# Kernel tuning notes

Measured on AMD Instinct MI355X. Metric: run time of the kernel, lower is better.

Reference implementation:

```python
import jax, jax.numpy as jnp
import numpy as np

TEMPERATURE = 0.5


def setup_inputs() -> dict:
    key = jax.random.key(0)
    k1, k2 = jax.random.split(key)
    N, Z = 4096, 2048
    z1 = jax.random.normal(k1, (N, Z), dtype=jnp.float32)
    z2 = jax.random.normal(k2, (N, Z), dtype=jnp.float32)
    return {"z1": z1, "z2": z2}


def reference(z1, z2):
    # NT-Xent loss. Original torch code: normalize, build full 2Nx2N cosine-sim
    # matrix, prepend the positive pair column, cross-entropy with label 0.
    # Mathematically, per-row CE with the positive prepended and the self-sim
    # removed equals: logsumexp over the row excluding the diagonal, minus the
    # positive logit.  (cosine_similarity on already-normalized vectors is a
    # plain dot product, so normalization is applied once.)
    n, _ = z1.shape
    a = z1 / jnp.linalg.norm(z1, axis=1, keepdims=True)  # [N, Z]
    b = z2 / jnp.linalg.norm(z2, axis=1, keepdims=True)  # [N, Z]
    reps = jnp.concatenate([a, b], axis=0)               # [2N, Z]
    logits = jnp.matmul(reps, reps.T) / TEMPERATURE      # [2N, 2N]
    NEG_INF = jnp.float32(-1e9)  # mask self-similarity (excluded from CE denom)
    logits = jnp.where(jnp.eye(2 * n, dtype=bool), NEG_INF, logits)
    pos = jnp.sum(a * b, axis=1) / TEMPERATURE           # [N] positive logits
    pos = jnp.concatenate([pos, pos])                    # [2N]
    lse = jax.nn.logsumexp(logits, axis=1)               # [2N]
    # sum of CE over 2N rows, divided by 2N  == mean
    return jnp.mean(lse - pos)
```

## Files before the change

### kernel.cpp

```cpp
#include <hip/hip_runtime.h>
#include <stdint.h>

#define N_ROWS 4096
#define Z_DIM  2048
#define TOT    8192
#define TILE   128
#define RBYTES (Z_DIM / 2)
#define BKE    256
#define KBYT   (BKE / 2)
#define NITER  (Z_DIM / BKE)
#define NT     (TOT / TILE)
#define NBLK   (NT * (NT + 1) / 2)
#define INV_T  2.0f
#define SCL4   64.0f

typedef __attribute__((ext_vector_type(4))) int   intx4;
typedef __attribute__((ext_vector_type(8))) int   intx8;
typedef __attribute__((ext_vector_type(4))) float floatx4;

__device__ __forceinline__ unsigned int f2fp4(float v) {
    float a = fabsf(v);
    unsigned int c = (a >= 0.25f) + (a >= 0.75f) + (a >= 1.25f) + (a >= 1.75f)
                   + (a >= 2.5f)  + (a >= 3.5f)  + (a >= 5.0f);
    return c | (v < 0.f ? 8u : 0u);
}

#define GLOAD16(g, l)                                                   \
    __builtin_amdgcn_global_load_lds(                                   \
        (const __attribute__((address_space(1))) unsigned int*)(g),     \
        (__attribute__((address_space(3))) unsigned int*)(l), 16, 0, 0)

__global__ __launch_bounds__(256) void normalize_kernel(
    const float* __restrict__ z1, const float* __restrict__ z2,
    unsigned char* __restrict__ reps, float* __restrict__ pos,
    float* __restrict__ rowsum)
{
    const int row  = blockIdx.x;
    const int tid  = threadIdx.x;
    const int lane = tid & 63, wave = tid >> 6;

    if (row < TOT / 256) rowsum[row * 256 + tid] = 0.f;

    const float4* p1 = (const float4*)(z1 + (size_t)row * Z_DIM);
    const float4* p2 = (const float4*)(z2 + (size_t)row * Z_DIM);
    float4 x0 = p1[tid * 2], x1 = p1[tid * 2 + 1];
    float4 y0 = p2[tid * 2], y1 = p2[tid * 2 + 1];

    float s1 = x0.x*x0.x + x0.y*x0.y + x0.z*x0.z + x0.w*x0.w
             + x1.x*x1.x + x1.y*x1.y + x1.z*x1.z + x1.w*x1.w;
    float s2 = y0.x*y0.x + y0.y*y0.y + y0.z*y0.z + y0.w*y0.w
             + y1.x*y1.x + y1.y*y1.y + y1.z*y1.z + y1.w*y1.w;
    float dd = x0.x*y0.x + x0.y*y0.y + x0.z*y0.z + x0.w*y0.w
             + x1.x*y1.x + x1.y*y1.y + x1.z*y1.z + x1.w*y1.w;

    #pragma unroll
    for (int m = 1; m < 64; m <<= 1) {
        s1 += __shfl_xor(s1, m);
        s2 += __shfl_xor(s2, m);
        dd += __shfl_xor(dd, m);
    }
    __shared__ float red[3][4];
    if (lane == 0) { red[0][wave] = s1; red[1][wave] = s2; red[2][wave] = dd; }
    __syncthreads();
    s1 = red[0][0] + red[0][1] + red[0][2] + red[0][3];
    s2 = red[1][0] + red[1][1] + red[1][2] + red[1][3];
    dd = red[2][0] + red[2][1] + red[2][2] + red[2][3];

    const float inv1 = rsqrtf(s1), inv2 = rsqrtf(s2);
    if (tid == 0) {
        float p = dd * inv1 * inv2 * INV_T;
        pos[row] = p;
        pos[row + N_ROWS] = p;
    }

    const float a = inv1 * SCL4, b = inv2 * SCL4;
    unsigned int pa =  f2fp4(x0.x * a)        | (f2fp4(x0.y * a) << 4)
                    | (f2fp4(x0.z * a) << 8)  | (f2fp4(x0.w * a) << 12)
                    | (f2fp4(x1.x * a) << 16) | (f2fp4(x1.y * a) << 20)
                    | (f2fp4(x1.z * a) << 24) | (f2fp4(x1.w * a) << 28);
    unsigned int pb =  f2fp4(y0.x * b)        | (f2fp4(y0.y * b) << 4)
                    | (f2fp4(y0.z * b) << 8)  | (f2fp4(y0.w * b) << 12)
                    | (f2fp4(y1.x * b) << 16) | (f2fp4(y1.y * b) << 20)
                    | (f2fp4(y1.z * b) << 24) | (f2fp4(y1.w * b) << 28);
    *(unsigned int*)(reps + (size_t)row * RBYTES + tid * 4) = pa;
    *(unsigned int*)(reps + (size_t)(N_ROWS + row) * RBYTES + tid * 4) = pb;
}

__global__ __launch_bounds__(256) void simclr_gemm(
    const unsigned char* __restrict__ reps, float* __restrict__ rowsum)
{
    __shared__ __align__(16) unsigned char L[2][2][16384];

    const int t = blockIdx.x;
    int r = (int)((sqrtf(8.0f * (float)t + 1.0f) - 1.0f) * 0.5f);
    while ((r + 1) * (r + 2) / 2 <= t) ++r;
    while (r * (r + 1) / 2 > t) --r;
    const int bi = t - r * (r + 1) / 2;
    const int bj = r;
    const bool diag = (bi == bj);

    const int tid  = threadIdx.x;
    const int lane = tid & 63, wave = tid >> 6;
    const int wr = wave >> 1, wc = wave & 1;
    const int quad = lane >> 4, l16 = lane & 15;
    const int sw   = l16 & 3;
    const int row0 = bi * TILE, col0 = bj * TILE;

    floatx4 acc[4][4];
    #pragma unroll
    for (int i = 0; i < 4; ++i)
        #pragma unroll
        for (int j = 0; j < 4; ++j)
            acc[i][j] = floatx4{0.f, 0.f, 0.f, 0.f};

    const int r_lo = tid >> 2, slot = tid & 3;
    const unsigned char* gA[4]; const unsigned char* gB[4]; int lofs[4];
    #pragma unroll
    for (int p = 0; p < 4; ++p) {
        const int rw = (p & 1) * 64 + r_lo;
        const int kc = (p >> 1) * 4 + (slot ^ (r_lo & 3));
        gA[p] = reps + (size_t)(row0 + rw) * RBYTES + kc * 16;
        gB[p] = reps + (size_t)(col0 + rw) * RBYTES + kc * 16;
        lofs[p] = p * 4096 + tid * 16;
    }

    #pragma unroll
    for (int p = 0; p < 4; ++p) GLOAD16(gA[p], &L[0][0][lofs[p]]);
    #pragma unroll
    for (int p = 0; p < 4; ++p) GLOAD16(gB[p], &L[0][1][lofs[p]]);
    __syncthreads();

    for (int i = 0; i < NITER; ++i) {
        if (i + 1 < NITER) {
            const size_t ko = (size_t)(i + 1) * KBYT;
            const int buf = (i + 1) & 1;
            #pragma unroll
            for (int p = 0; p < 4; ++p) GLOAD16(gA[p] + ko, &L[buf][0][lofs[p]]);
            #pragma unroll
            for (int p = 0; p < 4; ++p) GLOAD16(gB[p] + ko, &L[buf][1][lofs[p]]);
        }
        const unsigned char* Ab = &L[i & 1][0][0];
        const unsigned char* Bb = &L[i & 1][1][0];

        intx8 af[2][4], bf[2][4];
        #pragma unroll
        for (int h = 0; h < 2; ++h) {
            #pragma unroll
            for (int f = 0; f < 4; ++f) {
                const int ra = h * 8192 + (wr * 64 + f * 16 + l16) * 64 + ((quad ^ sw) << 4);
                const int rb = h * 8192 + (wc * 64 + f * 16 + l16) * 64 + ((quad ^ sw) << 4);
                intx4 av = *(const intx4*)&Ab[ra];
                intx4 bv = *(const intx4*)&Bb[rb];
                af[h][f] = intx8{av[0], av[1], av[2], av[3], 0, 0, 0, 0};
                bf[h][f] = intx8{bv[0], bv[1], bv[2], bv[3], 0, 0, 0, 0};
            }
        }
        #pragma unroll
        for (int h = 0; h < 2; ++h)
            #pragma unroll
            for (int fi = 0; fi < 4; ++fi)
                #pragma unroll
                for (int j = 0; j < 4; ++j)
                    acc[fi][j] = __builtin_amdgcn_mfma_scale_f32_16x16x128_f8f6f4(
                        af[h][fi], bf[h][j], acc[fi][j],
                        4, 4,
                        0, 0x7F7F7F7Fu,
                        0, 0x7F7F7F7Fu);
        __syncthreads();
    }

    const float descale = INV_T / (SCL4 * SCL4);
    float scol[4] = {0.f, 0.f, 0.f, 0.f};
    #pragma unroll
    for (int fi = 0; fi < 4; ++fi) {
        const int rbase = row0 + wr * 64 + fi * 16 + quad * 4;
        float srow[4] = {0.f, 0.f, 0.f, 0.f};
        #pragma unroll
        for (int j = 0; j < 4; ++j) {
            const int c = col0 + wc * 64 + j * 16 + l16;
            #pragma unroll
            for (int rr = 0; rr < 4; ++rr) {
                float e = __expf(acc[fi][j][rr] * descale);
                if (diag && (rbase + rr == c)) e = 0.f;
                srow[rr] += e;
                scol[j]  += e;
            }
        }
        #pragma unroll
        for (int rr = 0; rr < 4; ++rr) {
            #pragma unroll
            for (int m = 1; m < 16; m <<= 1) srow[rr] += __shfl_xor(srow[rr], m);
        }
        if (l16 == 0) {
            #pragma unroll
            for (int rr = 0; rr < 4; ++rr)
                atomicAdd(&rowsum[rbase + rr], srow[rr]);
        }
    }
    if (!diag) {
        #pragma unroll
        for (int j = 0; j < 4; ++j) {
            scol[j] += __shfl_xor(scol[j], 16);
            scol[j] += __shfl_xor(scol[j], 32);
        }
        if (quad == 0) {
            #pragma unroll
            for (int j = 0; j < 4; ++j)
                atomicAdd(&rowsum[col0 + wc * 64 + j * 16 + l16], scol[j]);
        }
    }
}

__global__ __launch_bounds__(1024) void finalize_kernel(
    const float* __restrict__ rowsum, const float* __restrict__ pos,
    float* __restrict__ out)
{
    const int tid = threadIdx.x;
    const int lane = tid & 63, wave = tid >> 6;
    float s = 0.f;
    for (int r = tid; r < TOT; r += 1024) s += logf(rowsum[r]) - pos[r];
    #pragma unroll
    for (int m = 1; m < 64; m <<= 1) s += __shfl_xor(s, m);
    __shared__ float red[16];
    if (lane == 0) red[wave] = s;
    __syncthreads();
    if (tid == 0) {
        float t = 0.f;
        #pragma unroll
        for (int w = 0; w < 16; ++w) t += red[w];
        out[0] = t * (1.0f / TOT);
    }
}

extern "C" void kernel_launch(void* const* d_in, const int* in_sizes, int n_in,
                              void* d_out, int out_size, void* d_ws, size_t ws_size,
                              hipStream_t stream)
{
    const float* z1 = (const float*)d_in[0];
    const float* z2 = (const float*)d_in[1];
    float* out = (float*)d_out;

    char* w = (char*)d_ws;
    unsigned char* reps = (unsigned char*)w;
    float* pos    = (float*)(w + (size_t)TOT * RBYTES);
    float* rowsum = pos + TOT;

    normalize_kernel<<<N_ROWS, 256, 0, stream>>>(z1, z2, reps, pos, rowsum);
    simclr_gemm<<<NBLK, 256, 0, stream>>>(reps, rowsum);
    finalize_kernel<<<1, 1024, 0, stream>>>(rowsum, pos, out);
}
```

Measured before the change: 157.2 us.

## Switch GEMM to 32x32x64 FP4 MFMA with two-wave blocks and smaller K-step

Replaces the 16x16x128 scaled FP4 MFMA tiles with 32x32x64 ones. Each block now has 2 waves instead of 4, each wave computing a 128x64 slab, and the LDS K-step is halved to 128 elements, which halves shared memory per block. The aim is fewer, larger MFMA instructions with better operand reuse, and more resident blocks per CU. The cost is more accumulator registers per wave, twice as many K iterations and barriers, and a wider row reduction in the epilogue (16 values reduced across 32 lanes).

Result: slower. 188.8 us (+20.1%).

```diff
diff --git a/kernel.cpp b/kernel.cpp
--- a/kernel.cpp
+++ b/kernel.cpp
@@ -6,7 +6,7 @@
 #define TOT    8192
 #define TILE   128
 #define RBYTES (Z_DIM / 2)
-#define BKE    256
+#define BKE    128
 #define KBYT   (BKE / 2)
 #define NITER  (Z_DIM / BKE)
 #define NT     (TOT / TILE)
@@ -14,9 +14,9 @@
 #define INV_T  2.0f
 #define SCL4   64.0f
 
-typedef __attribute__((ext_vector_type(4))) int   intx4;
-typedef __attribute__((ext_vector_type(8))) int   intx8;
-typedef __attribute__((ext_vector_type(4))) float floatx4;
+typedef __attribute__((ext_vector_type(4)))  int   intx4;
+typedef __attribute__((ext_vector_type(8)))  int   intx8;
+typedef __attribute__((ext_vector_type(16))) float floatx16;
 
 __device__ __forceinline__ unsigned int f2fp4(float v) {
     float a = fabsf(v);
@@ -86,10 +86,10 @@
     *(unsigned int*)(reps + (size_t)(N_ROWS + row) * RBYTES + tid * 4) = pb;
 }
 
-__global__ __launch_bounds__(256) void simclr_gemm(
+__global__ __launch_bounds__(128) void simclr_gemm(
     const unsigned char* __restrict__ reps, float* __restrict__ rowsum)
 {
-    __shared__ __align__(16) unsigned char L[2][2][16384];
+    __shared__ __align__(16) unsigned char L[2][2][8192];
 
     const int t = blockIdx.x;
     int r = (int)((sqrtf(8.0f * (float)t + 1.0f) - 1.0f) * 0.5f);
@@ -101,33 +101,31 @@
 
     const int tid  = threadIdx.x;
     const int lane = tid & 63, wave = tid >> 6;
-    const int wr = wave >> 1, wc = wave & 1;
-    const int quad = lane >> 4, l16 = lane & 15;
-    const int sw   = l16 & 3;
+    const int l32  = lane & 31, half = lane >> 5;
     const int row0 = bi * TILE, col0 = bj * TILE;
 
-    floatx4 acc[4][4];
+    floatx16 acc[4][2];
     #pragma unroll
     for (int i = 0; i < 4; ++i)
         #pragma unroll
-        for (int j = 0; j < 4; ++j)
-            acc[i][j] = floatx4{0.f, 0.f, 0.f, 0.f};
-
-    const int r_lo = tid >> 2, slot = tid & 3;
+        for (int j = 0; j < 2; ++j)
+            #pragma unroll
+            for (int e = 0; e < 16; ++e) acc[i][j][e] = 0.f;
+
     const unsigned char* gA[4]; const unsigned char* gB[4]; int lofs[4];
     #pragma unroll
-    for (int p = 0; p < 4; ++p) {
-        const int rw = (p & 1) * 64 + r_lo;
-        const int kc = (p >> 1) * 4 + (slot ^ (r_lo & 3));
-        gA[p] = reps + (size_t)(row0 + rw) * RBYTES + kc * 16;
-        gB[p] = reps + (size_t)(col0 + rw) * RBYTES + kc * 16;
-        lofs[p] = p * 4096 + tid * 16;
-    }
-
-    #pragma unroll
-    for (int p = 0; p < 4; ++p) GLOAD16(gA[p], &L[0][0][lofs[p]]);
-    #pragma unroll
-    for (int p = 0; p < 4; ++p) GLOAD16(gB[p], &L[0][1][lofs[p]]);
+    for (int q = 0; q < 4; ++q) {
+        const int c = q * 128 + tid;
+        const int srow = c >> 2, gkc = (c & 3) ^ (srow & 3);
+        gA[q] = reps + (size_t)(row0 + srow) * RBYTES + gkc * 16;
+        gB[q] = reps + (size_t)(col0 + srow) * RBYTES + gkc * 16;
+        lofs[q] = c * 16;
+    }
+
+    #pragma unroll
+    for (int q = 0; q < 4; ++q) GLOAD16(gA[q], &L[0][0][lofs[q]]);
+    #pragma unroll
+    for (int q = 0; q < 4; ++q) GLOAD16(gB[q], &L[0][1][lofs[q]]);
     __syncthreads();
 
     for (int i = 0; i < NITER; ++i) {
@@ -135,78 +133,77 @@
             const size_t ko = (size_t)(i + 1) * KBYT;
             const int buf = (i + 1) & 1;
             #pragma unroll
-            for (int p = 0; p < 4; ++p) GLOAD16(gA[p] + ko, &L[buf][0][lofs[p]]);
-            #pragma unroll
-            for (int p = 0; p < 4; ++p) GLOAD16(gB[p] + ko, &L[buf][1][lofs[p]]);
+            for (int q = 0; q < 4; ++q) GLOAD16(gA[q] + ko, &L[buf][0][lofs[q]]);
+            #pragma unroll
+            for (int q = 0; q < 4; ++q) GLOAD16(gB[q] + ko, &L[buf][1][lofs[q]]);
         }
         const unsigned char* Ab = &L[i & 1][0][0];
         const unsigned char* Bb = &L[i & 1][1][0];
 
-        intx8 af[2][4], bf[2][4];
-        #pragma unroll
-        for (int h = 0; h < 2; ++h) {
-            #pragma unroll
-            for (int f = 0; f < 4; ++f) {
-                const int ra = h * 8192 + (wr * 64 + f * 16 + l16) * 64 + ((quad ^ sw) << 4);
-                const int rb = h * 8192 + (wc * 64 + f * 16 + l16) * 64 + ((quad ^ sw) << 4);
-                intx4 av = *(const intx4*)&Ab[ra];
-                intx4 bv = *(const intx4*)&Bb[rb];
-                af[h][f] = intx8{av[0], av[1], av[2], av[3], 0, 0, 0, 0};
-                bf[h][f] = intx8{bv[0], bv[1], bv[2], bv[3], 0, 0, 0, 0};
+        #pragma unroll
+        for (int s = 0; s < 2; ++s) {
+            const int kchunk = s * 2 + half;
+            intx8 bfr[2];
+            #pragma unroll
+            for (int j = 0; j < 2; ++j) {
+                const int br = wave * 64 + j * 32 + l32;
+                intx4 bv = *(const intx4*)&Bb[br * 64 + ((kchunk ^ (br & 3)) << 4)];
+                bfr[j] = intx8{bv[0], bv[1], bv[2], bv[3], 0, 0, 0, 0};
             }
-        }
-        #pragma unroll
-        for (int h = 0; h < 2; ++h)
-            #pragma unroll
-            for (int fi = 0; fi < 4; ++fi)
+            #pragma unroll
+            for (int fi = 0; fi < 4; ++fi) {
+                const int ar = fi * 32 + l32;
+                intx4 av = *(const intx4*)&Ab[ar * 64 + ((kchunk ^ (ar & 3)) << 4)];
+                intx8 afr = intx8{av[0], av[1], av[2], av[3], 0, 0, 0, 0};
                 #pragma unroll
-                for (int j = 0; j < 4; ++j)
-                    acc[fi][j] = __builtin_amdgcn_mfma_scale_f32_16x16x128_f8f6f4(
-                        af[h][fi], bf[h][j], acc[fi][j],
+                for (int j = 0; j < 2; ++j)
+                    acc[fi][j] = __builtin_amdgcn_mfma_scale_f32_32x32x64_f8f6f4(
+                        afr, bfr[j], acc[fi][j],
                         4, 4,
                         0, 0x7F7F7F7Fu,
                         0, 0x7F7F7F7Fu);
+            }
+        }
         __syncthreads();
     }
 
     const float descale = INV_T / (SCL4 * SCL4);
-    float scol[4] = {0.f, 0.f, 0.f, 0.f};
+    float scol[2] = {0.f, 0.f};
     #pragma unroll
     for (int fi = 0; fi < 4; ++fi) {
-        const int rbase = row0 + wr * 64 + fi * 16 + quad * 4;
-        float srow[4] = {0.f, 0.f, 0.f, 0.f};
-        #pragma unroll
-        for (int j = 0; j < 4; ++j) {
-            const int c = col0 + wc * 64 + j * 16 + l16;
-            #pragma unroll
-            for (int rr = 0; rr < 4; ++rr) {
-                float e = __expf(acc[fi][j][rr] * descale);
-                if (diag && (rbase + rr == c)) e = 0.f;
-                srow[rr] += e;
-                scol[j]  += e;
+        float srow[16];
+        #pragma unroll
+        for (int e = 0; e < 16; ++e) srow[e] = 0.f;
+        #pragma unroll
+        for (int j = 0; j < 2; ++j) {
+            const int c = col0 + wave * 64 + j * 32 + l32;
+            #pragma unroll
+            for (int e = 0; e < 16; ++e) {
+                const int rw = row0 + fi * 32 + (e & 3) + 8 * (e >> 2) + 4 * half;
+                float v = __expf(acc[fi][j][e] * descale);
+                if (diag && (rw == c)) v = 0.f;
+                srow[e] += v;
+                scol[j] += v;
             }
         }
         #pragma unroll
-        for (int rr = 0; rr < 4; ++rr) {
-            #pragma unroll
-            for (int m = 1; m < 16; m <<= 1) srow[rr] += __shfl_xor(srow[rr], m);
-        }
-        if (l16 == 0) {
-            #pragma unroll
-            for (int rr = 0; rr < 4; ++rr)
-                atomicAdd(&rowsum[rbase + rr], srow[rr]);
+        for (int e = 0; e < 16; ++e) {
+            #pragma unroll
+            for (int m = 1; m < 32; m <<= 1) srow[e] += __shfl_xor(srow[e], m);
+        }
+        if (l32 == 0) {
+            #pragma unroll
+            for (int e = 0; e < 16; ++e)
+                atomicAdd(&rowsum[row0 + fi * 32 + (e & 3) + 8 * (e >> 2) + 4 * half],
+                          srow[e]);
         }
     }
     if (!diag) {
         #pragma unroll
-        for (int j = 0; j < 4; ++j) {
-            scol[j] += __shfl_xor(scol[j], 16);
+        for (int j = 0; j < 2; ++j) {
             scol[j] += __shfl_xor(scol[j], 32);
-        }
-        if (quad == 0) {
-            #pragma unroll
-            for (int j = 0; j < 4; ++j)
-                atomicAdd(&rowsum[col0 + wc * 64 + j * 16 + l16], scol[j]);
+            if (half == 0)
+                atomicAdd(&rowsum[col0 + wave * 64 + j * 32 + l32], scol[j]);
         }
     }
 }
@@ -246,6 +243,6 @@
     float* rowsum = pos + TOT;
 
     normalize_kernel<<<N_ROWS, 256, 0, stream>>>(z1, z2, reps, pos, rowsum);
-    simclr_gemm<<<NBLK, 256, 0, stream>>>(reps, rowsum);
+    simclr_gemm<<<NBLK, 128, 0, stream>>>(reps, rowsum);
     finalize_kernel<<<1, 1024, 0, stream>>>(rowsum, pos, out);
 }
```
